# Kernel tuning notes

Hardware: AMD Instinct MI355X
Metric: run time of the kernel (lower is better)

Reference implementation:

```python
import jax, jax.numpy as jnp
import numpy as np
from jax.scipy.special import gammaln

# dims: S=state_dim, A=act_dim, H=horizon, HY=hyper_dim, B=batch, T=seq len
S, A, H, HY, B, T = 256, 16, 30, 64, 64, 64
EPS = 1e-6


def setup_inputs() -> dict:
    key = jax.random.key(0)
    ks = jax.random.split(key, 9)
    logp_o = jax.nn.log_softmax(jax.random.normal(ks[0], (T, B, S)), axis=-1)
    logp_u = jax.nn.log_softmax(jax.random.normal(ks[1], (T, B, A)), axis=-1)
    value = jax.random.normal(ks[2], (H, B, A, S))
    z = jax.random.normal(ks[3], (B, HY))
    b = jax.nn.softmax(jax.random.normal(ks[4], (B, S)), axis=-1)
    # learned parameters (xavier-ish scales, matching torch init magnitudes)
    w = jax.random.normal(ks[5], (1, A, S, S)) * (2.0 / (S + S)) ** 0.5
    w_offset_w = jax.random.normal(ks[6], (A * S * S, HY)) * 0.01  # Linear weight * 0.1
    tau = jax.random.uniform(ks[7], (1, 1), minval=-1.0, maxval=1.0)
    tau_offset_w = jax.random.normal(ks[8], (1, HY)) * 0.01
    return {"logp_o": logp_o, "logp_u": logp_u, "value": value, "z": z, "b": b,
            "w": w, "w_offset_w": w_offset_w, "tau": tau, "tau_offset_w": tau_offset_w}


def rectify(x):
    # positive rate; clipped exp for numerical safety
    return jnp.exp(jnp.clip(x, -8.0, 8.0))


def poisson_pdf(rate, K):
    # truncated, renormalized Poisson pmf over horizons 1..K; rate: [B,1] -> [B,K]
    ks = jnp.arange(1, K + 1, dtype=rate.dtype)
    logp = ks * jnp.log(rate) - rate - gammaln(ks + 1.0)
    return jax.nn.softmax(logp, axis=-1)


def reference(logp_o, logp_u, value, z, b, w, w_offset_w, tau, tau_offset_w):
    # compute_transition: hyper-offset + base full-rank weights, softmax over next-state
    w_off = (z @ w_offset_w.T).reshape(B, A, S, S)
    transition = jax.nn.softmax(w_off + w, axis=-1)  # [B,A,S,S]

    # compute_horizon_dist
    rate = rectify(tau + z @ tau_offset_w.T)  # [B,1]
    h_dist = poisson_pdf(rate, H)             # [B,H]

    # update_action for all timesteps at once
    alpha_a = jax.nn.softmax(logp_u, axis=-1)  # [T,B,A]

    def plan(b_t):
        # [B,S] x [H,B,A,S] -> [H,B,A]
        logits = jnp.einsum('bi,hbki->hbk', b_t, value)
        a = jax.nn.softmax(logits, axis=-1)
        return jnp.einsum('hbk,bh->bk', a, h_dist)  # [B,A]

    def step(b_t, inp):
        lo_t, a_t = inp
        # update_belief
        s_next = jnp.einsum('bkij,bi,bk->bj', transition, b_t, a_t)  # [B,S]
        b_next = jax.nn.softmax(jnp.log(s_next + EPS) + lo_t, axis=-1)
        return b_next, (b_next, plan(b_next))

    _, (alpha_b, alpha_pi) = jax.lax.scan(step, b, (logp_o, alpha_a))
    return alpha_b, alpha_pi  # [T,B,S], [T,B,A]
```

## Files before the change

kernel.cpp:

```cpp
#include <hip/hip_runtime.h>
#include <hip/hip_fp16.h>

#define DS 256
#define DA 16
#define DH 30
#define DHY 64
#define DB 64
#define DT 64

union HV  { int4 i4; __half2 h2[4]; };
union HV2 { int2 i2; __half2 h2[2]; };
typedef _Float16 f16x8 __attribute__((ext_vector_type(8)));
typedef float f32x4 __attribute__((ext_vector_type(4)));

__global__ __launch_bounds__(256) void k_setup(const float* __restrict__ z,
                                               const float* __restrict__ tau,
                                               const float* __restrict__ tauw,
                                               const float* __restrict__ logp_u,
                                               const float* __restrict__ value,
                                               float* __restrict__ h_dist,
                                               _Float16* __restrict__ zf,
                                               float* __restrict__ alpha_a,
                                               __half* __restrict__ v16, int n4) {
  const int wg = blockIdx.x;
  if (wg == 0) {
    const int bb = threadIdx.x;
    if (bb >= DB) return;
    float x = tau[0];
    for (int hy = 0; hy < DHY; ++hy) x = fmaf(z[bb * DHY + hy], tauw[hy], x);
    x = fminf(fmaxf(x, -8.f), 8.f);
    const float rate = __expf(x);
    const float lr = x;
    float lp[DH];
    float lg = 0.f;
    float mx = -1e30f;
    #pragma unroll
    for (int h = 0; h < DH; ++h) {
      const float ks = (float)(h + 1);
      lg += __logf(ks);
      lp[h] = ks * lr - rate - lg;
      mx = fmaxf(mx, lp[h]);
    }
    float sum = 0.f;
    #pragma unroll
    for (int h = 0; h < DH; ++h) { lp[h] = __expf(lp[h] - mx); sum += lp[h]; }
    const float inv = 1.f / sum;
    #pragma unroll
    for (int h = 0; h < DH; ++h) h_dist[bb * DH + h] = lp[h] * inv;
  } else if (wg < 17) {
    const int i = (wg - 1) * 256 + threadIdx.x;
    if (i < DB * DHY) zf[i] = (_Float16)z[i];
  } else if (wg < 273) {
    const int row = (wg - 17) * 16 + (threadIdx.x >> 4);
    const int k = threadIdx.x & 15;
    const float v = logp_u[(size_t)row * DA + k];
    float m = v;
    #pragma unroll
    for (int o = 8; o >= 1; o >>= 1) m = fmaxf(m, __shfl_xor(m, o, 16));
    const float e = __expf(v - m);
    float s = e;
    #pragma unroll
    for (int o = 8; o >= 1; o >>= 1) s += __shfl_xor(s, o, 16);
    alpha_a[(size_t)row * DA + k] = e / s;
  } else {
    const int stride = 1024 * 256;
    for (int i = (wg - 273) * 256 + threadIdx.x; i < n4; i += stride) {
      const float4 f = reinterpret_cast<const float4*>(value)[i];
      reinterpret_cast<__half2*>(v16)[2 * i]     = __floats2half2_rn(f.x, f.y);
      reinterpret_cast<__half2*>(v16)[2 * i + 1] = __floats2half2_rn(f.z, f.w);
    }
  }
}

__global__ __launch_bounds__(256) void k_zero(float* __restrict__ out_pi) {
  out_pi[blockIdx.x * 256 + threadIdx.x] = 0.f;
}

__global__ __launch_bounds__(256) void k_trans(const float* __restrict__ w,
                                               const float* __restrict__ wofs,
                                               const _Float16* __restrict__ zf,
                                               __half* __restrict__ trans) {
  const int ki = blockIdx.x;
  const int t = threadIdx.x;
  const int l = t & 63;
  const int wv = t >> 6;
  __shared__ __align__(16) char smem[32 * 1024];

  {
    const float* wrow = wofs + (size_t)ki * (DS * DHY);
    const int q = t & 3;
    #pragma unroll
    for (int pass = 0; pass < 4; ++pass) {
      const int j = pass * 64 + (t >> 2);
      const float4* src = reinterpret_cast<const float4*>(wrow + (size_t)j * DHY + q * 16);
      const float4 f0 = src[0], f1 = src[1], f2 = src[2], f3 = src[3];
      __half2 h[8];
      h[0] = __floats2half2_rn(f0.x, f0.y); h[1] = __floats2half2_rn(f0.z, f0.w);
      h[2] = __floats2half2_rn(f1.x, f1.y); h[3] = __floats2half2_rn(f1.z, f1.w);
      h[4] = __floats2half2_rn(f2.x, f2.y); h[5] = __floats2half2_rn(f2.z, f2.w);
      h[6] = __floats2half2_rn(f3.x, f3.y); h[7] = __floats2half2_rn(f3.z, f3.w);
      const int4* hv = reinterpret_cast<const int4*>(h);
      int b0 = j * 128 + (q * 2) * 16;     b0 ^= ((j & 7) << 4);
      int b1 = j * 128 + (q * 2 + 1) * 16; b1 ^= ((j & 7) << 4);
      *reinterpret_cast<int4*>(smem + b0) = hv[0];
      *reinterpret_cast<int4*>(smem + b1) = hv[1];
    }
  }
  __syncthreads();

  const int bcol = wv * 16 + (l & 15);
  const f16x8 Bf0 = *reinterpret_cast<const f16x8*>(zf + bcol * DHY + 0  + (l >> 4) * 8);
  const f16x8 Bf1 = *reinterpret_cast<const f16x8*>(zf + bcol * DHY + 32 + (l >> 4) * 8);

  f32x4 acc[16];
  #pragma unroll
  for (int m = 0; m < 16; ++m) {
    const int row0 = m * 16 + (l >> 4) * 4;
    const float4 w4 = *reinterpret_cast<const float4*>(w + (size_t)ki * DS + row0);
    acc[m][0] = w4.x; acc[m][1] = w4.y; acc[m][2] = w4.z; acc[m][3] = w4.w;
  }
  #pragma unroll
  for (int m = 0; m < 16; ++m) {
    const int row = m * 16 + (l & 15);
    int ba = row * 128 + (l >> 4) * 16;        ba ^= ((row & 7) << 4);
    int bb = row * 128 + (4 + (l >> 4)) * 16;  bb ^= ((row & 7) << 4);
    const f16x8 a0 = *reinterpret_cast<const f16x8*>(smem + ba);
    const f16x8 a1 = *reinterpret_cast<const f16x8*>(smem + bb);
    acc[m] = __builtin_amdgcn_mfma_f32_16x16x32_f16(a0, Bf0, acc[m], 0, 0, 0);
    acc[m] = __builtin_amdgcn_mfma_f32_16x16x32_f16(a1, Bf1, acc[m], 0, 0, 0);
  }

  float ssum = 0.f;
  #pragma unroll
  for (int m = 0; m < 16; ++m) {
    acc[m][0] = __expf(acc[m][0]); acc[m][1] = __expf(acc[m][1]);
    acc[m][2] = __expf(acc[m][2]); acc[m][3] = __expf(acc[m][3]);
    ssum += (acc[m][0] + acc[m][1]) + (acc[m][2] + acc[m][3]);
  }
  ssum += __shfl_xor(ssum, 16, 64);
  ssum += __shfl_xor(ssum, 32, 64);
  const float inv = 1.f / ssum;

  __half* tb = trans + (size_t)bcol * (DA * DS * DS) + (size_t)ki * DS;
  #pragma unroll
  for (int m = 0; m < 16; ++m) {
    const int j0 = m * 16 + (l >> 4) * 4;
    union { int2 i2; __half2 h[2]; } o;
    o.h[0] = __floats2half2_rn(acc[m][0] * inv, acc[m][1] * inv);
    o.h[1] = __floats2half2_rn(acc[m][2] * inv, acc[m][3] * inv);
    *reinterpret_cast<int2*>(tb + j0) = o.i2;
  }
}

__global__ __launch_bounds__(256) void k_mbuild(const __half* __restrict__ trans,
                                                const float* __restrict__ alpha_a,
                                                __half* __restrict__ Mch,
                                                int t0, int TC) {
  const int b = blockIdx.x >> 4;
  const int ich = (blockIdx.x & 15) << 4;
  const int tid = threadIdx.x;
  const int lane = tid & 63;
  const int wid = tid >> 6;
  __shared__ __half2 a_lds[16 * DA];
  for (int r = tid; r < TC * DA; r += 256)
    a_lds[r] = __float2half2_rn(alpha_a[((size_t)(t0 + (r >> 4)) * DB + b) * DA + (r & 15)]);
  __syncthreads();
  for (int io = 0; io < 4; ++io) {
    const int i = ich + io * 4 + wid;
    const __half* tp = trans + ((size_t)b * DA * DS + i) * DS + lane * 4;
    __half2 T2[32];
    #pragma unroll
    for (int k = 0; k < 16; ++k) {
      HV2 u;
      u.i2 = *reinterpret_cast<const int2*>(tp + (size_t)k * (DS * DS));
      T2[2 * k]     = u.h2[0];
      T2[2 * k + 1] = u.h2[1];
    }
    const __half2 z2 = __float2half2_rn(0.f);
    for (int tt = 0; tt < TC; ++tt) {
      __half2 m0 = z2, m1 = z2;
      #pragma unroll
      for (int k = 0; k < 16; ++k) {
        const __half2 ak = a_lds[tt * DA + k];
        m0 = __hfma2(ak, T2[2 * k], m0);
        m1 = __hfma2(ak, T2[2 * k + 1], m1);
      }
      HV2 o;
      o.h2[0] = m0;
      o.h2[1] = m1;
      *reinterpret_cast<int2*>(Mch + (((size_t)tt * DB + b) * DS + i) * DS + lane * 4) = o.i2;
    }
  }
}

#define LBAR() asm volatile("s_waitcnt lgkmcnt(0)\n\ts_barrier" ::: "memory")

#define SC_ISSUE(S, T)                                                          \
  if ((T) < TC) {                                                               \
    const __half* mb_ = Mch + (((size_t)(T) * DB + b) << 16) + jg * 8;          \
    S##0 = *reinterpret_cast<const int4*>(mb_ + (size_t)(iq + 0 * 32) * DS);    \
    S##1 = *reinterpret_cast<const int4*>(mb_ + (size_t)(iq + 1 * 32) * DS);    \
    S##2 = *reinterpret_cast<const int4*>(mb_ + (size_t)(iq + 2 * 32) * DS);    \
    S##3 = *reinterpret_cast<const int4*>(mb_ + (size_t)(iq + 3 * 32) * DS);    \
    S##4 = *reinterpret_cast<const int4*>(mb_ + (size_t)(iq + 4 * 32) * DS);    \
    S##5 = *reinterpret_cast<const int4*>(mb_ + (size_t)(iq + 5 * 32) * DS);    \
    S##6 = *reinterpret_cast<const int4*>(mb_ + (size_t)(iq + 6 * 32) * DS);    \
    S##7 = *reinterpret_cast<const int4*>(mb_ + (size_t)(iq + 7 * 32) * DS);    \
    if (tid < 64) lo_##S = *reinterpret_cast<const float4*>(                    \
        logp_o + ((size_t)(t0 + (T)) * DB + b) * DS + tid * 4);                 \
  }

#define SC_ACC1(Q, IT) {                                                 \
    const float wgt = bl[(IT) * 32 + iq];                                \
    HV u; u.i4 = (Q);                                                    \
    const float2 f0 = __half22float2(u.h2[0]);                           \
    const float2 f1 = __half22float2(u.h2[1]);                           \
    const float2 f2 = __half22float2(u.h2[2]);                           \
    const float2 f3 = __half22float2(u.h2[3]);                           \
    acc0 = fmaf(wgt, f0.x, acc0); acc1 = fmaf(wgt, f0.y, acc1);          \
    acc2 = fmaf(wgt, f1.x, acc2); acc3 = fmaf(wgt, f1.y, acc3);          \
    acc4 = fmaf(wgt, f2.x, acc4); acc5 = fmaf(wgt, f2.y, acc5);          \
    acc6 = fmaf(wgt, f3.x, acc6); acc7 = fmaf(wgt, f3.y, acc7); }

#define SC_STEP(S, T) {                                                  \
    float acc0=0.f,acc1=0.f,acc2=0.f,acc3=0.f,acc4=0.f,acc5=0.f,acc6=0.f,acc7=0.f; \
    SC_ACC1(S##0, 0) SC_ACC1(S##1, 1) SC_ACC1(S##2, 2) SC_ACC1(S##3, 3)  \
    SC_ACC1(S##4, 4) SC_ACC1(S##5, 5) SC_ACC1(S##6, 6) SC_ACC1(S##7, 7)  \
    acc0 += __shfl_xor(acc0, 32, 64); acc1 += __shfl_xor(acc1, 32, 64);  \
    acc2 += __shfl_xor(acc2, 32, 64); acc3 += __shfl_xor(acc3, 32, 64);  \
    acc4 += __shfl_xor(acc4, 32, 64); acc5 += __shfl_xor(acc5, 32, 64);  \
    acc6 += __shfl_xor(acc6, 32, 64); acc7 += __shfl_xor(acc7, 32, 64);  \
    if (lane < 32) {                                                     \
      red[w][lane][0] = acc0; red[w][lane][1] = acc1;                    \
      red[w][lane][2] = acc2; red[w][lane][3] = acc3;                    \
      red[w][lane][4] = acc4; red[w][lane][5] = acc5;                    \
      red[w][lane][6] = acc6; red[w][lane][7] = acc7;                    \
    }                                                                    \
    const float4 loC = lo_##S;   \
    LBAR();                                  \
    SC_ISSUE(S, (T) + 2)                \
    if (tid < 64) {                                                      \
      const int jj = tid >> 1, q0 = (tid & 1) * 4;                       \
      float4 sv = {0.f, 0.f, 0.f, 0.f};                                  \
      _Pragma("unroll")                                                  \
      for (int w2 = 0; w2 < 16; ++w2) {                                  \
        const float4 r4 = *reinterpret_cast<const float4*>(&red[w2][jj][q0]); \
        sv.x += r4.x; sv.y += r4.y; sv.z += r4.z; sv.w += r4.w;          \
      }                                                                  \
      const float e0 = __expf(__logf(sv.x + 1e-6f) + loC.x);             \
      const float e1 = __expf(__logf(sv.y + 1e-6f) + loC.y);             \
      const float e2 = __expf(__logf(sv.z + 1e-6f) + loC.z);             \
      const float e3 = __expf(__logf(sv.w + 1e-6f) + loC.w);             \
      float ps = (e0 + e1) + (e2 + e3);                                  \
      ps += __shfl_xor(ps, 1, 64);  ps += __shfl_xor(ps, 2, 64);         \
      ps += __shfl_xor(ps, 4, 64);  ps += __shfl_xor(ps, 8, 64);         \
      ps += __shfl_xor(ps, 16, 64); ps += __shfl_xor(ps, 32, 64);        \
      const float inv = 1.f / ps;                                        \
      float4 p4;                                                         \
      p4.x = e0 * inv; p4.y = e1 * inv; p4.z = e2 * inv; p4.w = e3 * inv;\
      *reinterpret_cast<float4*>(&bl[tid * 4]) = p4;                     \
      *reinterpret_cast<float4*>(                                        \
          &out_b[((size_t)(t0 + (T)) * DB + b) * DS + tid * 4]) = p4;    \
    }                                                                    \
    LBAR();   }

__global__ __launch_bounds__(1024, 4) void k_scanchunk(
    const __half* __restrict__ Mch,
    const float* __restrict__ logp_o,
    const float* __restrict__ b0,
    float* __restrict__ bl_buf,
    float* __restrict__ out_b,
    int t0, int TC) {
  const int b = blockIdx.x;
  const int tid = threadIdx.x;
  const int lane = tid & 63;
  const int w = tid >> 6;
  const int jg = tid & 31;
  const int iq = tid >> 5;
  __shared__ __align__(16) float bl[DS];
  __shared__ __align__(16) float red[16][32][12];
  if (tid < DS) bl[tid] = (t0 == 0) ? b0[b * DS + tid] : bl_buf[b * DS + tid];
  __syncthreads();

  int4 A0, A1, A2, A3, A4, A5, A6, A7;
  int4 B0, B1, B2, B3, B4, B5, B6, B7;
  float4 lo_A = {0.f, 0.f, 0.f, 0.f}, lo_B = {0.f, 0.f, 0.f, 0.f};

  SC_ISSUE(A, 0)
  SC_ISSUE(B, 1)
  for (int tt = 0; tt < TC; tt += 2) {
    SC_STEP(A, tt)
    SC_STEP(B, tt + 1)
  }
  if (tid < DS) bl_buf[b * DS + tid] = bl[tid];
}

__global__ __launch_bounds__(256) void k_planall(const float* __restrict__ out_b,
                                                 const __half* __restrict__ value16,
                                                 const float* __restrict__ h_dist,
                                                 float* __restrict__ out_pi) {
  const int b = blockIdx.x >> 6;
  const int t = blockIdx.x & 63;
  const int tid = threadIdx.x;
  const int lane = tid & 63;
  const int wid = tid >> 6;
  __shared__ __align__(16) float bl[DS];
  __shared__ float api[DA];
  bl[tid] = out_b[((size_t)t * DB + b) * DS + tid];
  if (tid < DA) api[tid] = 0.f;
  __syncthreads();
  const int k = lane >> 2;
  const int q = lane & 3;
  for (int p = 0; p < 8; ++p) {
    const int h = p * 4 + wid;
    if (h < DH) {
      const __half* vr = value16 + (((size_t)h * DB + b) * DA + k) * DS + q * 64;
      const float* blq = bl + q * 64;
      float dot = 0.f;
      #pragma unroll
      for (int ii = 0; ii < 64; ii += 8) {
        HV u;
        u.i4 = *reinterpret_cast<const int4*>(vr + ii);
        const float4 c0 = *reinterpret_cast<const float4*>(blq + ii);
        const float4 c1 = *reinterpret_cast<const float4*>(blq + ii + 4);
        const float2 f0 = __half22float2(u.h2[0]);
        const float2 f1 = __half22float2(u.h2[1]);
        const float2 f2 = __half22float2(u.h2[2]);
        const float2 f3 = __half22float2(u.h2[3]);
        dot = fmaf(f0.x, c0.x, dot); dot = fmaf(f0.y, c0.y, dot);
        dot = fmaf(f1.x, c0.z, dot); dot = fmaf(f1.y, c0.w, dot);
        dot = fmaf(f2.x, c1.x, dot); dot = fmaf(f2.y, c1.y, dot);
        dot = fmaf(f3.x, c1.z, dot); dot = fmaf(f3.y, c1.w, dot);
      }
      dot += __shfl_xor(dot, 1, 64);
      dot += __shfl_xor(dot, 2, 64);
      float mk = dot;
      #pragma unroll
      for (int o = 4; o <= 32; o <<= 1) mk = fmaxf(mk, __shfl_xor(mk, o, 64));
      const float ek = __expf(dot - mk);
      float sk = ek;
      #pragma unroll
      for (int o = 4; o <= 32; o <<= 1) sk += __shfl_xor(sk, o, 64);
      if (q == 0) atomicAdd(&api[k], (ek / sk) * h_dist[b * DH + h]);
    }
  }
  __syncthreads();
  if (tid < DA) out_pi[((size_t)t * DB + b) * DA + tid] = api[tid];
}

#define K_LD(I) (*reinterpret_cast<const int4*>(tb + (size_t)((I) * 64 + rb) * DS))
#define K_FMA(QV, I) {                                              \
    HV u; u.i4 = (QV);                                              \
    const float wgt = wv[(I) * 64 + rb];                            \
    const float2 f0 = __half22float2(u.h2[0]);                      \
    const float2 f1 = __half22float2(u.h2[1]);                      \
    const float2 f2 = __half22float2(u.h2[2]);                      \
    const float2 f3 = __half22float2(u.h2[3]);                      \
    acc[0] = fmaf(wgt, f0.x, acc[0]); acc[1] = fmaf(wgt, f0.y, acc[1]); \
    acc[2] = fmaf(wgt, f1.x, acc[2]); acc[3] = fmaf(wgt, f1.y, acc[3]); \
    acc[4] = fmaf(wgt, f2.x, acc[4]); acc[5] = fmaf(wgt, f2.y, acc[5]); \
    acc[6] = fmaf(wgt, f3.x, acc[6]); acc[7] = fmaf(wgt, f3.y, acc[7]); }

__global__ __launch_bounds__(256, 2) void k_step(
    const __half* __restrict__ trans, const float* __restrict__ logp_o,
    const float* __restrict__ logp_u, const __half* __restrict__ value16,
    const float* __restrict__ h_dist, const float* __restrict__ b0,
    float* __restrict__ s_buf, float* __restrict__ out_b,
    float* __restrict__ out_pi, int t) {
  const int bb = blockIdx.x & 63;
  const int jt = blockIdx.x >> 6;
  const int tid = threadIdx.x;
  const int lane = tid & 63;
  const int wid = tid >> 6;
  __shared__ __align__(16) float wv[DA * DS];
  __shared__ __align__(16) float bl[DS];
  __shared__ float aa[DA];
  __shared__ float redm[4], reds[4];
  __shared__ float red4[4][4][8];
  __shared__ float api[DA];
  if (t > 0) {
    const int tp = t - 1;
    const float sv = s_buf[(size_t)(tp & 1) * DB * DS + bb * DS + tid];
    const float l = __logf(sv + 1e-6f) + logp_o[((size_t)tp * DB + bb) * DS + tid];
    float m = l;
    #pragma unroll
    for (int o = 32; o >= 1; o >>= 1) m = fmaxf(m, __shfl_xor(m, o, 64));
    if (lane == 0) redm[wid] = m;
    __syncthreads();
    m = fmaxf(fmaxf(redm[0], redm[1]), fmaxf(redm[2], redm[3]));
    const float e = __expf(l - m);
    float v = e;
    #pragma unroll
    for (int o = 32; o >= 1; o >>= 1) v += __shfl_xor(v, o, 64);
    if (lane == 0) reds[wid] = v;
    if (tid < DA) api[tid] = 0.f;
    __syncthreads();
    const float p = e / (reds[0] + reds[1] + reds[2] + reds[3]);
    bl[tid] = p;
    if (jt == 0) out_b[((size_t)tp * DB + bb) * DS + tid] = p;
    __syncthreads();
    const int h = jt * 4 + wid;
    const int k = lane >> 2;
    const int q = lane & 3;
    if (h < DH) {
      const __half* vr = value16 + (((size_t)h * DB + bb) * DA + k) * DS + q * 64;
      const float* blq = bl + q * 64;
      float dot = 0.f;
      #pragma unroll
      for (int ii = 0; ii < 64; ii += 8) {
        HV u;
        u.i4 = *reinterpret_cast<const int4*>(vr + ii);
        const float4 c0 = *reinterpret_cast<const float4*>(blq + ii);
        const float4 c1 = *reinterpret_cast<const float4*>(blq + ii + 4);
        const float2 f0 = __half22float2(u.h2[0]);
        const float2 f1 = __half22float2(u.h2[1]);
        const float2 f2 = __half22float2(u.h2[2]);
        const float2 f3 = __half22float2(u.h2[3]);
        dot = fmaf(f0.x, c0.x, dot); dot = fmaf(f0.y, c0.y, dot);
        dot = fmaf(f1.x, c0.z, dot); dot = fmaf(f1.y, c0.w, dot);
        dot = fmaf(f2.x, c1.x, dot); dot = fmaf(f2.y, c1.y, dot);
        dot = fmaf(f3.x, c1.z, dot); dot = fmaf(f3.y, c1.w, dot);
      }
      dot += __shfl_xor(dot, 1, 64);
      dot += __shfl_xor(dot, 2, 64);
      float mk = dot;
      #pragma unroll
      for (int o = 4; o <= 32; o <<= 1) mk = fmaxf(mk, __shfl_xor(mk, o, 64));
      const float ek = __expf(dot - mk);
      float sk = ek;
      #pragma unroll
      for (int o = 4; o <= 32; o <<= 1) sk += __shfl_xor(sk, o, 64);
      if (q == 0) atomicAdd(&api[k], (ek / sk) * h_dist[bb * DH + h]);
    }
    __syncthreads();
    if (tid < DA) atomicAdd(&out_pi[((size_t)tp * DB + bb) * DA + tid], api[tid]);
  } else {
    bl[tid] = b0[bb * DS + tid];
  }
  __syncthreads();
  if (t < DT) {
    if (tid < DA) {
      const float lg = logp_u[((size_t)t * DB + bb) * DA + tid];
      float m = lg;
      #pragma unroll
      for (int o = 8; o >= 1; o >>= 1) m = fmaxf(m, __shfl_xor(m, o, 16));
      const float e = __expf(lg - m);
      float s = e;
      #pragma unroll
      for (int o = 8; o >= 1; o >>= 1) s += __shfl_xor(s, o, 16);
      aa[tid] = e / s;
    }
    __syncthreads();
    #pragma unroll
    for (int r = tid; r < DA * DS; r += 256) wv[r] = aa[r >> 8] * bl[r & 255];
    __syncthreads();
    const int jg = tid & 3;
    const int rb = tid >> 2;
    const __half* tb = trans + (size_t)bb * (DA * DS * DS) + jt * 32 + jg * 8;
    float acc[8] = {0.f, 0.f, 0.f, 0.f, 0.f, 0.f, 0.f, 0.f};
    int4 Q0 = K_LD(0), Q1 = K_LD(1), Q2 = K_LD(2), Q3 = K_LD(3);
    int4 Q4 = K_LD(4), Q5 = K_LD(5), Q6 = K_LD(6), Q7 = K_LD(7);
    #pragma unroll
    for (int it = 0; it < 56; it += 8) {
      K_FMA(Q0, it + 0); Q0 = K_LD(it + 8);
      K_FMA(Q1, it + 1); Q1 = K_LD(it + 9);
      K_FMA(Q2, it + 2); Q2 = K_LD(it + 10);
      K_FMA(Q3, it + 3); Q3 = K_LD(it + 11);
      K_FMA(Q4, it + 4); Q4 = K_LD(it + 12);
      K_FMA(Q5, it + 5); Q5 = K_LD(it + 13);
      K_FMA(Q6, it + 6); Q6 = K_LD(it + 14);
      K_FMA(Q7, it + 7); Q7 = K_LD(it + 15);
    }
    K_FMA(Q0, 56); K_FMA(Q1, 57); K_FMA(Q2, 58); K_FMA(Q3, 59);
    K_FMA(Q4, 60); K_FMA(Q5, 61); K_FMA(Q6, 62); K_FMA(Q7, 63);
    #pragma unroll
    for (int q = 0; q < 8; ++q) {
      acc[q] += __shfl_xor(acc[q], 4, 64);
      acc[q] += __shfl_xor(acc[q], 8, 64);
      acc[q] += __shfl_xor(acc[q], 16, 64);
      acc[q] += __shfl_xor(acc[q], 32, 64);
    }
    if (lane < 4) {
      #pragma unroll
      for (int q = 0; q < 8; ++q) red4[wid][lane][q] = acc[q];
    }
    __syncthreads();
    if (tid < 32) {
      const int jg2 = tid >> 3, q2 = tid & 7;
      const float s = red4[0][jg2][q2] + red4[1][jg2][q2] +
                      red4[2][jg2][q2] + red4[3][jg2][q2];
      s_buf[(size_t)(t & 1) * DB * DS + bb * DS + jt * 32 + jg2 * 8 + q2] = s;
    }
  }
}


extern "C" void kernel_launch(void* const* d_in, const int* in_sizes, int n_in,
                              void* d_out, int out_size, void* d_ws, size_t ws_size,
                              hipStream_t stream) {
  const float* logp_o = (const float*)d_in[0];
  const float* logp_u = (const float*)d_in[1];
  const float* value  = (const float*)d_in[2];
  const float* z      = (const float*)d_in[3];
  const float* b0     = (const float*)d_in[4];
  const float* w      = (const float*)d_in[5];
  const float* wofs   = (const float*)d_in[6];
  const float* tau    = (const float*)d_in[7];
  const float* tauw   = (const float*)d_in[8];

  char* ws = (char*)d_ws;
  size_t off = 0;
  __half* trans    = (__half*)(ws + off);    off += (size_t)DB * DA * DS * DS * sizeof(__half);
  __half* value16  = (__half*)(ws + off);    off += (size_t)DH * DB * DA * DS * sizeof(__half);
  float* alpha_a   = (float*)(ws + off);     off += (size_t)DT * DB * DA * sizeof(float);
  float* s_buf     = (float*)(ws + off);     off += (size_t)2 * DB * DS * sizeof(float);
  float* bl_buf    = (float*)(ws + off);     off += (size_t)DB * DS * sizeof(float);
  _Float16* zf16   = (_Float16*)(ws + off);  off += (size_t)DB * DHY * sizeof(_Float16);
  float* h_dist    = (float*)(ws + off);     off += 8192;
  const size_t base = off;
  if (base > ws_size) return;
  __half* M = (__half*)(ws + base);
  const size_t m_per_t = (size_t)DB * DS * DS * sizeof(__half);
  int TC = 0;
  const int cands[4] = {16, 8, 4, 2};
  for (int c = 0; c < 4; ++c)
    if (base + (size_t)cands[c] * m_per_t <= ws_size) { TC = cands[c]; break; }

  float* out_b  = (float*)d_out;
  float* out_pi = out_b + (size_t)DT * DB * DS;

  k_setup<<<1297, 256, 0, stream>>>(z, tau, tauw, logp_u, value,
                                    h_dist, zf16, alpha_a, value16,
                                    DH * DB * DA * DS / 4);
  k_trans<<<DA * DS, 256, 0, stream>>>(w, wofs, zf16, trans);

  if (TC) {
    for (int c = 0; c < DT / TC; ++c) {
      k_mbuild<<<DB * 16, 256, 0, stream>>>(trans, alpha_a, M, c * TC, TC);
      k_scanchunk<<<DB, 1024, 0, stream>>>(M, logp_o, b0, bl_buf, out_b, c * TC, TC);
    }
    k_planall<<<DT * DB, 256, 0, stream>>>(out_b, value16, h_dist, out_pi);
  } else {
    k_zero<<<256, 256, 0, stream>>>(out_pi);
    for (int t = 0; t <= DT; ++t) {
      k_step<<<512, 256, 0, stream>>>(trans, logp_o, logp_u, value16, h_dist, b0,
                                      s_buf, out_b, out_pi, t);
    }
  }
}
```

Before: 596.5 us.

## Fuse plan computation into scan launches, overlapping previous chunk planning

Adds a k_scanplan kernel. Its first 64 blocks run the belief-scan chunk, and 128 extra blocks compute the planning softmax for the previously finished 16-step chunk. This lets the plan work run alongside the latency-bound scan and removes the separate k_planall launch. The scan loop is also fully unrolled with a fixed chunk of 16. The per-step k_step fallback is removed. The issue guard is now hardcoded to 16, so the smaller-chunk fallback path could read past valid M entries.

```diff
diff --git a/kernel.cpp b/kernel.cpp
--- a/kernel.cpp
+++ b/kernel.cpp
@@ -196,7 +196,7 @@
 #define LBAR() asm volatile("s_waitcnt lgkmcnt(0)\n\ts_barrier" ::: "memory")
 
 #define SC_ISSUE(S, T)                                                          \
-  if ((T) < TC) {                                                               \
+  if ((T) < 16) {                                                               \
     const __half* mb_ = Mch + (((size_t)(T) * DB + b) << 16) + jg * 8;          \
     S##0 = *reinterpret_cast<const int4*>(mb_ + (size_t)(iq + 0 * 32) * DS);    \
     S##1 = *reinterpret_cast<const int4*>(mb_ + (size_t)(iq + 1 * 32) * DS);    \
@@ -236,9 +236,9 @@
       red[w][lane][4] = acc4; red[w][lane][5] = acc5;                    \
       red[w][lane][6] = acc6; red[w][lane][7] = acc7;                    \
     }                                                                    \
-    const float4 loC = lo_##S;   \
-    LBAR();                                  \
-    SC_ISSUE(S, (T) + 2)                \
+    const float4 loC = lo_##S;                                           \
+    LBAR();                                                              \
+    SC_ISSUE(S, (T) + 2)                                                 \
     if (tid < 64) {                                                      \
       const int jj = tid >> 1, q0 = (tid & 1) * 4;                       \
       float4 sv = {0.f, 0.f, 0.f, 0.f};                                  \
@@ -262,7 +262,100 @@
       *reinterpret_cast<float4*>(                                        \
           &out_b[((size_t)(t0 + (T)) * DB + b) * DS + tid * 4]) = p4;    \
     }                                                                    \
-    LBAR();   }
+    LBAR(); }
+
+__global__ __launch_bounds__(1024, 4) void k_scanplan(
+    const __half* __restrict__ Mch,
+    const float* __restrict__ logp_o,
+    const float* __restrict__ b0,
+    const __half* __restrict__ value16,
+    const float* __restrict__ h_dist,
+    float* __restrict__ bl_buf,
+    float* __restrict__ out_b,
+    float* __restrict__ out_pi,
+    int t0, int cplan_t0) {
+  const int wg = blockIdx.x;
+  const int tid = threadIdx.x;
+  const int lane = tid & 63;
+  const int w = tid >> 6;
+
+  __shared__ __align__(16) float bl[DS];
+  __shared__ __align__(16) float red[16][32][12];
+  __shared__ __align__(16) float bl4[4][DS];
+  __shared__ float api4[4][DA];
+
+  if (wg < 64) {
+    if (t0 >= DT) return;
+    const int b = wg;
+    const int jg = tid & 31;
+    const int iq = tid >> 5;
+    if (tid < DS) bl[tid] = (t0 == 0) ? b0[b * DS + tid] : bl_buf[b * DS + tid];
+    __syncthreads();
+    int4 A0, A1, A2, A3, A4, A5, A6, A7;
+    int4 B0, B1, B2, B3, B4, B5, B6, B7;
+    float4 lo_A = {0.f, 0.f, 0.f, 0.f}, lo_B = {0.f, 0.f, 0.f, 0.f};
+    SC_ISSUE(A, 0)
+    SC_ISSUE(B, 1)
+    #pragma unroll
+    for (int tt = 0; tt < 16; tt += 2) {
+      SC_STEP(A, tt)
+      SC_STEP(B, tt + 1)
+    }
+    if (tid < DS) bl_buf[b * DS + tid] = bl[tid];
+  } else {
+    if (cplan_t0 < 0) return;
+    const int sub = tid >> 8;
+    const int tid2 = tid & 255;
+    const int wid2 = tid2 >> 6;
+    const int k = lane >> 2;
+    const int q = lane & 3;
+    #pragma unroll 1
+    for (int e = 0; e < 2; ++e) {
+      const int p = ((wg - 64) * 4 + sub) * 2 + e;
+      const int b = p >> 4;
+      const int t = cplan_t0 + (p & 15);
+      bl4[sub][tid2] = out_b[((size_t)t * DB + b) * DS + tid2];
+      if (tid2 < DA) api4[sub][tid2] = 0.f;
+      __syncthreads();
+      for (int pp = 0; pp < 8; ++pp) {
+        const int h = pp * 4 + wid2;
+        if (h < DH) {
+          const __half* vr = value16 + (((size_t)h * DB + b) * DA + k) * DS + q * 64;
+          const float* blq = &bl4[sub][q * 64];
+          float dot = 0.f;
+          #pragma unroll
+          for (int ii = 0; ii < 64; ii += 8) {
+            HV u;
+            u.i4 = *reinterpret_cast<const int4*>(vr + ii);
+            const float4 c0 = *reinterpret_cast<const float4*>(blq + ii);
+            const float4 c1 = *reinterpret_cast<const float4*>(blq + ii + 4);
+            const float2 f0 = __half22float2(u.h2[0]);
+            const float2 f1 = __half22float2(u.h2[1]);
+            const float2 f2 = __half22float2(u.h2[2]);
+            const float2 f3 = __half22float2(u.h2[3]);
+            dot = fmaf(f0.x, c0.x, dot); dot = fmaf(f0.y, c0.y, dot);
+            dot = fmaf(f1.x, c0.z, dot); dot = fmaf(f1.y, c0.w, dot);
+            dot = fmaf(f2.x, c1.x, dot); dot = fmaf(f2.y, c1.y, dot);
+            dot = fmaf(f3.x, c1.z, dot); dot = fmaf(f3.y, c1.w, dot);
+          }
+          dot += __shfl_xor(dot, 1, 64);
+          dot += __shfl_xor(dot, 2, 64);
+          float mk = dot;
+          #pragma unroll
+          for (int o = 4; o <= 32; o <<= 1) mk = fmaxf(mk, __shfl_xor(mk, o, 64));
+          const float ek = __expf(dot - mk);
+          float sk = ek;
+          #pragma unroll
+          for (int o = 4; o <= 32; o <<= 1) sk += __shfl_xor(sk, o, 64);
+          if (q == 0) atomicAdd(&api4[sub][k], (ek / sk) * h_dist[b * DH + h]);
+        }
+      }
+      __syncthreads();
+      if (tid2 < DA) out_pi[((size_t)t * DB + b) * DA + tid2] = api4[sub][tid2];
+      __syncthreads();
+    }
+  }
+}
 
 __global__ __launch_bounds__(1024, 4) void k_scanchunk(
     const __half* __restrict__ Mch,
@@ -281,11 +374,10 @@
   __shared__ __align__(16) float red[16][32][12];
   if (tid < DS) bl[tid] = (t0 == 0) ? b0[b * DS + tid] : bl_buf[b * DS + tid];
   __syncthreads();
-
   int4 A0, A1, A2, A3, A4, A5, A6, A7;
   int4 B0, B1, B2, B3, B4, B5, B6, B7;
   float4 lo_A = {0.f, 0.f, 0.f, 0.f}, lo_B = {0.f, 0.f, 0.f, 0.f};
-
+  #define SC_TC TC
   SC_ISSUE(A, 0)
   SC_ISSUE(B, 1)
   for (int tt = 0; tt < TC; tt += 2) {
@@ -348,152 +440,6 @@
   if (tid < DA) out_pi[((size_t)t * DB + b) * DA + tid] = api[tid];
 }
 
-#define K_LD(I) (*reinterpret_cast<const int4*>(tb + (size_t)((I) * 64 + rb) * DS))
-#define K_FMA(QV, I) {                                              \
-    HV u; u.i4 = (QV);                                              \
-    const float wgt = wv[(I) * 64 + rb];                            \
-    const float2 f0 = __half22float2(u.h2[0]);                      \
-    const float2 f1 = __half22float2(u.h2[1]);                      \
-    const float2 f2 = __half22float2(u.h2[2]);                      \
-    const float2 f3 = __half22float2(u.h2[3]);                      \
-    acc[0] = fmaf(wgt, f0.x, acc[0]); acc[1] = fmaf(wgt, f0.y, acc[1]); \
-    acc[2] = fmaf(wgt, f1.x, acc[2]); acc[3] = fmaf(wgt, f1.y, acc[3]); \
-    acc[4] = fmaf(wgt, f2.x, acc[4]); acc[5] = fmaf(wgt, f2.y, acc[5]); \
-    acc[6] = fmaf(wgt, f3.x, acc[6]); acc[7] = fmaf(wgt, f3.y, acc[7]); }
-
-__global__ __launch_bounds__(256, 2) void k_step(
-    const __half* __restrict__ trans, const float* __restrict__ logp_o,
-    const float* __restrict__ logp_u, const __half* __restrict__ value16,
-    const float* __restrict__ h_dist, const float* __restrict__ b0,
-    float* __restrict__ s_buf, float* __restrict__ out_b,
-    float* __restrict__ out_pi, int t) {
-  const int bb = blockIdx.x & 63;
-  const int jt = blockIdx.x >> 6;
-  const int tid = threadIdx.x;
-  const int lane = tid & 63;
-  const int wid = tid >> 6;
-  __shared__ __align__(16) float wv[DA * DS];
-  __shared__ __align__(16) float bl[DS];
-  __shared__ float aa[DA];
-  __shared__ float redm[4], reds[4];
-  __shared__ float red4[4][4][8];
-  __shared__ float api[DA];
-  if (t > 0) {
-    const int tp = t - 1;
-    const float sv = s_buf[(size_t)(tp & 1) * DB * DS + bb * DS + tid];
-    const float l = __logf(sv + 1e-6f) + logp_o[((size_t)tp * DB + bb) * DS + tid];
-    float m = l;
-    #pragma unroll
-    for (int o = 32; o >= 1; o >>= 1) m = fmaxf(m, __shfl_xor(m, o, 64));
-    if (lane == 0) redm[wid] = m;
-    __syncthreads();
-    m = fmaxf(fmaxf(redm[0], redm[1]), fmaxf(redm[2], redm[3]));
-    const float e = __expf(l - m);
-    float v = e;
-    #pragma unroll
-    for (int o = 32; o >= 1; o >>= 1) v += __shfl_xor(v, o, 64);
-    if (lane == 0) reds[wid] = v;
-    if (tid < DA) api[tid] = 0.f;
-    __syncthreads();
-    const float p = e / (reds[0] + reds[1] + reds[2] + reds[3]);
-    bl[tid] = p;
-    if (jt == 0) out_b[((size_t)tp * DB + bb) * DS + tid] = p;
-    __syncthreads();
-    const int h = jt * 4 + wid;
-    const int k = lane >> 2;
-    const int q = lane & 3;
-    if (h < DH) {
-      const __half* vr = value16 + (((size_t)h * DB + bb) * DA + k) * DS + q * 64;
-      const float* blq = bl + q * 64;
-      float dot = 0.f;
-      #pragma unroll
-      for (int ii = 0; ii < 64; ii += 8) {
-        HV u;
-        u.i4 = *reinterpret_cast<const int4*>(vr + ii);
-        const float4 c0 = *reinterpret_cast<const float4*>(blq + ii);
-        const float4 c1 = *reinterpret_cast<const float4*>(blq + ii + 4);
-        const float2 f0 = __half22float2(u.h2[0]);
-        const float2 f1 = __half22float2(u.h2[1]);
-        const float2 f2 = __half22float2(u.h2[2]);
-        const float2 f3 = __half22float2(u.h2[3]);
-        dot = fmaf(f0.x, c0.x, dot); dot = fmaf(f0.y, c0.y, dot);
-        dot = fmaf(f1.x, c0.z, dot); dot = fmaf(f1.y, c0.w, dot);
-        dot = fmaf(f2.x, c1.x, dot); dot = fmaf(f2.y, c1.y, dot);
-        dot = fmaf(f3.x, c1.z, dot); dot = fmaf(f3.y, c1.w, dot);
-      }
-      dot += __shfl_xor(dot, 1, 64);
-      dot += __shfl_xor(dot, 2, 64);
-      float mk = dot;
-      #pragma unroll
-      for (int o = 4; o <= 32; o <<= 1) mk = fmaxf(mk, __shfl_xor(mk, o, 64));
-      const float ek = __expf(dot - mk);
-      float sk = ek;
-      #pragma unroll
-      for (int o = 4; o <= 32; o <<= 1) sk += __shfl_xor(sk, o, 64);
-      if (q == 0) atomicAdd(&api[k], (ek / sk) * h_dist[bb * DH + h]);
-    }
-    __syncthreads();
-    if (tid < DA) atomicAdd(&out_pi[((size_t)tp * DB + bb) * DA + tid], api[tid]);
-  } else {
-    bl[tid] = b0[bb * DS + tid];
-  }
-  __syncthreads();
-  if (t < DT) {
-    if (tid < DA) {
-      const float lg = logp_u[((size_t)t * DB + bb) * DA + tid];
-      float m = lg;
-      #pragma unroll
-      for (int o = 8; o >= 1; o >>= 1) m = fmaxf(m, __shfl_xor(m, o, 16));
-      const float e = __expf(lg - m);
-      float s = e;
-      #pragma unroll
-      for (int o = 8; o >= 1; o >>= 1) s += __shfl_xor(s, o, 16);
-      aa[tid] = e / s;
-    }
-    __syncthreads();
-    #pragma unroll
-    for (int r = tid; r < DA * DS; r += 256) wv[r] = aa[r >> 8] * bl[r & 255];
-    __syncthreads();
-    const int jg = tid & 3;
-    const int rb = tid >> 2;
-    const __half* tb = trans + (size_t)bb * (DA * DS * DS) + jt * 32 + jg * 8;
-    float acc[8] = {0.f, 0.f, 0.f, 0.f, 0.f, 0.f, 0.f, 0.f};
-    int4 Q0 = K_LD(0), Q1 = K_LD(1), Q2 = K_LD(2), Q3 = K_LD(3);
-    int4 Q4 = K_LD(4), Q5 = K_LD(5), Q6 = K_LD(6), Q7 = K_LD(7);
-    #pragma unroll
-    for (int it = 0; it < 56; it += 8) {
-      K_FMA(Q0, it + 0); Q0 = K_LD(it + 8);
-      K_FMA(Q1, it + 1); Q1 = K_LD(it + 9);
-      K_FMA(Q2, it + 2); Q2 = K_LD(it + 10);
-      K_FMA(Q3, it + 3); Q3 = K_LD(it + 11);
-      K_FMA(Q4, it + 4); Q4 = K_LD(it + 12);
-      K_FMA(Q5, it + 5); Q5 = K_LD(it + 13);
-      K_FMA(Q6, it + 6); Q6 = K_LD(it + 14);
-      K_FMA(Q7, it + 7); Q7 = K_LD(it + 15);
-    }
-    K_FMA(Q0, 56); K_FMA(Q1, 57); K_FMA(Q2, 58); K_FMA(Q3, 59);
-    K_FMA(Q4, 60); K_FMA(Q5, 61); K_FMA(Q6, 62); K_FMA(Q7, 63);
-    #pragma unroll
-    for (int q = 0; q < 8; ++q) {
-      acc[q] += __shfl_xor(acc[q], 4, 64);
-      acc[q] += __shfl_xor(acc[q], 8, 64);
-      acc[q] += __shfl_xor(acc[q], 16, 64);
-      acc[q] += __shfl_xor(acc[q], 32, 64);
-    }
-    if (lane < 4) {
-      #pragma unroll
-      for (int q = 0; q < 8; ++q) red4[wid][lane][q] = acc[q];
-    }
-    __syncthreads();
-    if (tid < 32) {
-      const int jg2 = tid >> 3, q2 = tid & 7;
-      const float s = red4[0][jg2][q2] + red4[1][jg2][q2] +
-                      red4[2][jg2][q2] + red4[3][jg2][q2];
-      s_buf[(size_t)(t & 1) * DB * DS + bb * DS + jt * 32 + jg2 * 8 + q2] = s;
-    }
-  }
-}
-
 
 extern "C" void kernel_launch(void* const* d_in, const int* in_sizes, int n_in,
                               void* d_out, int out_size, void* d_ws, size_t ws_size,
@@ -513,7 +459,6 @@
   __half* trans    = (__half*)(ws + off);    off += (size_t)DB * DA * DS * DS * sizeof(__half);
   __half* value16  = (__half*)(ws + off);    off += (size_t)DH * DB * DA * DS * sizeof(__half);
   float* alpha_a   = (float*)(ws + off);     off += (size_t)DT * DB * DA * sizeof(float);
-  float* s_buf     = (float*)(ws + off);     off += (size_t)2 * DB * DS * sizeof(float);
   float* bl_buf    = (float*)(ws + off);     off += (size_t)DB * DS * sizeof(float);
   _Float16* zf16   = (_Float16*)(ws + off);  off += (size_t)DB * DHY * sizeof(_Float16);
   float* h_dist    = (float*)(ws + off);     off += 8192;
@@ -534,17 +479,18 @@
                                     DH * DB * DA * DS / 4);
   k_trans<<<DA * DS, 256, 0, stream>>>(w, wofs, zf16, trans);
 
-  if (TC) {
+  if (TC == 16) {
+    for (int c = 0; c < 5; ++c) {
+      if (c < 4) k_mbuild<<<DB * 16, 256, 0, stream>>>(trans, alpha_a, M, c * 16, 16);
+      k_scanplan<<<192, 1024, 0, stream>>>(M, logp_o, b0, value16, h_dist,
+                                           bl_buf, out_b, out_pi,
+                                           c * 16, (c - 1) * 16);
+    }
+  } else if (TC) {
     for (int c = 0; c < DT / TC; ++c) {
       k_mbuild<<<DB * 16, 256, 0, stream>>>(trans, alpha_a, M, c * TC, TC);
       k_scanchunk<<<DB, 1024, 0, stream>>>(M, logp_o, b0, bl_buf, out_b, c * TC, TC);
     }
     k_planall<<<DT * DB, 256, 0, stream>>>(out_b, value16, h_dist, out_pi);
-  } else {
-    k_zero<<<256, 256, 0, stream>>>(out_pi);
-    for (int t = 0; t <= DT; ++t) {
-      k_step<<<512, 256, 0, stream>>>(trans, logp_o, logp_u, value16, h_dist, b0,
-                                      s_buf, out_b, out_pi, t);
-    }
-  }
-}
+  }
+}
```

Measured after the change: 607.3 us. No clear change (+1.8%).
